# Optimization experiments

Measured on AMD Instinct MI355X. Metric: run time of the kernel, lower is better.

The kernel has to match this reference:

```python
import jax, jax.numpy as jnp
import numpy as np

N = 50000
E = 800000
D = 128          # in_dim == hidden_dim
EDGE_DIM = 1
H = 128          # hidden_dim


def setup_inputs() -> dict:
    key = jax.random.key(0)
    ks = jax.random.split(key, 16)
    inp = {
        "x": jax.random.normal(ks[0], (N, D), jnp.float32),
        "pos": jax.random.normal(ks[1], (N, 3), jnp.float32),
        "edge_index": jax.random.randint(ks[2], (2, E), 0, N, jnp.int64),
        "edge_attr": jax.random.normal(ks[3], (E, EDGE_DIM), jnp.float32),
        "s": jax.random.uniform(ks[4], (N,), jnp.float32),
    }
    # edge_mlp: Linear(2D+1+edge_dim -> H), SiLU, Linear(H -> H), SiLU
    e_in = 2 * D + 1 + EDGE_DIM
    def lin(k, fan_in, fan_out):
        lim = 1.0 / np.sqrt(fan_in)
        kw, kb = jax.random.split(k)
        W = jax.random.uniform(kw, (fan_in, fan_out), jnp.float32, -lim, lim)
        b = jax.random.uniform(kb, (fan_out,), jnp.float32, -lim, lim)
        return W, b
    inp["W_e1"], inp["b_e1"] = lin(ks[5], e_in, H)
    inp["W_e2"], inp["b_e2"] = lin(ks[6], H, H)
    # node_mlp: Linear(D+H -> H), SiLU, Linear(H -> D)
    inp["W_n1"], inp["b_n1"] = lin(ks[7], D + H, H)
    inp["W_n2"], inp["b_n2"] = lin(ks[8], H, D)
    # coord_mlp: Linear(H -> 1)
    inp["W_c"], inp["b_c"] = lin(ks[9], H, 1)
    return inp


def reference(x, pos, edge_index, edge_attr, s,
              W_e1, b_e1, W_e2, b_e2, W_n1, b_n1, W_n2, b_n2, W_c, b_c):
    src, dst = edge_index[0], edge_index[1]
    n = x.shape[0]

    # edge gather + relative geometry
    diff = pos[dst] - pos[src]                      # [E, 3]
    r2 = jnp.sum(diff * diff, axis=-1, keepdims=True)  # [E, 1]
    e_in = jnp.concatenate([x[dst], x[src], r2, edge_attr], axis=-1)  # [E, 2D+1+edge_dim]

    # edge MLP
    m = jax.nn.silu(e_in @ W_e1 + b_e1)
    m = jax.nn.silu(m @ W_e2 + b_e2)                # [E, H]

    # s-gate on source nodes
    m = m * s[src][:, None]

    # scatter-add aggregation with degree normalization
    m_sum = jax.ops.segment_sum(m, dst, num_segments=n)          # [N, H]
    deg = jax.ops.segment_sum(jnp.ones((m.shape[0], 1), m.dtype), dst, num_segments=n)
    deg = jnp.maximum(deg, 1.0)
    m_sum = m_sum / deg

    # node update
    h = jax.nn.silu(jnp.concatenate([x, m_sum], axis=-1) @ W_n1 + b_n1)
    x_out = h @ W_n2 + b_n2                         # [N, D]

    # coordinate update
    gamma = m @ W_c + b_c                           # [E, 1]
    coord_update = jax.ops.segment_sum(gamma * diff, dst, num_segments=n) / deg
    pos_out = pos + coord_update                    # [N, 3]
    return x_out, pos_out
```

## Files before the change

### kernel.cpp

```cpp
#include <hip/hip_runtime.h>
#include <hip/hip_bf16.h>

#define NN 50000
#define EE 800000
#define SCAN_BLOCKS 196

typedef __bf16 bf16x8_t __attribute__((ext_vector_type(8)));
typedef float f32x4_t __attribute__((ext_vector_type(4)));

__device__ __forceinline__ float silu_f(float v) {
    return v * __builtin_amdgcn_rcpf(1.0f + __expf(-v));
}

__global__ void prep_kernel(const float* __restrict__ x,
                            const float* __restrict__ We1,
                            const float* __restrict__ We2,
                            const float* __restrict__ Wn1,
                            const float* __restrict__ Wn2,
                            const int* __restrict__ eidx,
                            __bf16* __restrict__ xb,
                            __bf16* __restrict__ WyS,
                            __bf16* __restrict__ We2S,
                            __bf16* __restrict__ Wn1T,
                            __bf16* __restrict__ Wn2T,
                            int* __restrict__ hist) {
    int tid = blockIdx.x * blockDim.x + threadIdx.x;
    int np = gridDim.x * blockDim.x;
    const int NX = NN * 128 / 4;
    for (int i = tid; i < NX; i += np) {
        float4 v = ((const float4*)x)[i];
        __bf16* o = xb + (size_t)i * 4;
        o[0] = (__bf16)v.x; o[1] = (__bf16)v.y; o[2] = (__bf16)v.z; o[3] = (__bf16)v.w;
    }
    for (int i = tid; i < 256 * 128; i += np) {
        int k = i >> 7, n = i & 127;
        int h = (k < 128) ? n : (128 + n);
        int k2 = k & 127;
        WyS[(k2 >> 5) * 8192 + h * 32 + (k2 & 31)] = (__bf16)We1[i];
        Wn1T[n * 256 + k] = (__bf16)Wn1[i];
    }
    for (int i = tid; i < 128 * 128; i += np) {
        int k = i >> 7, n = i & 127;
        We2S[(k >> 5) * 4096 + n * 32 + (k & 31)] = (__bf16)We2[i];
        Wn2T[n * 128 + k] = (__bf16)Wn2[i];
    }
    for (int i = tid; i < EE; i += np) {
        atomicAdd(&hist[eidx[EE + i]], 1);
    }
}

__global__ __launch_bounds__(256, 4)
void ygemm_kernel(const __bf16* __restrict__ xb,
                  const __bf16* __restrict__ WyS,
                  float* __restrict__ y) {
    __shared__ __align__(16) __bf16 Abf[64 * 136];
    __shared__ __align__(16) __bf16 Wy[256 * 32];

    const int t = threadIdx.x;
    const int r0 = blockIdx.x * 64;
    const int w = t >> 6;
    const int lane = t & 63;
    const int m_ = lane & 15;
    const int q = lane >> 4;

#pragma unroll
    for (int i = 0; i < 4; ++i) {
        int id = t + 256 * i;
        int rl = id >> 4, c8 = (id & 15) * 8;
        int row = r0 + rl;
        uint4 v = (row < NN) ? *(const uint4*)(xb + (long)row * 128 + c8)
                             : make_uint4(0, 0, 0, 0);
        *(uint4*)(Abf + rl * 136 + c8) = v;
    }

    f32x4_t acc[16];
#pragma unroll
    for (int ct = 0; ct < 16; ++ct) acc[ct] = (f32x4_t){0.f, 0.f, 0.f, 0.f};

    const int wrow = t >> 2;
    const int pch = (t & 3) ^ ((wrow >> 1) & 3);
    const int wofs = wrow * 32 + pch * 8;
    const int rofs = m_ * 32 + (q ^ ((m_ >> 1) & 3)) * 8;

    uint4 v0 = *(const uint4*)(WyS + t * 8);
    uint4 v1 = *(const uint4*)(WyS + 2048 + t * 8);
    uint4 v2 = *(const uint4*)(WyS + 4096 + t * 8);
    uint4 v3 = *(const uint4*)(WyS + 6144 + t * 8);
#pragma unroll
    for (int ks = 0; ks < 4; ++ks) {
        __syncthreads();
        *(uint4*)(Wy + wofs) = v0;
        *(uint4*)(Wy + 64 * 32 + wofs) = v1;
        *(uint4*)(Wy + 128 * 32 + wofs) = v2;
        *(uint4*)(Wy + 192 * 32 + wofs) = v3;
        __syncthreads();
        if (ks < 3) {
            v0 = *(const uint4*)(WyS + (ks + 1) * 8192 + t * 8);
            v1 = *(const uint4*)(WyS + (ks + 1) * 8192 + 2048 + t * 8);
            v2 = *(const uint4*)(WyS + (ks + 1) * 8192 + 4096 + t * 8);
            v3 = *(const uint4*)(WyS + (ks + 1) * 8192 + 6144 + t * 8);
        }
        bf16x8_t a = *(const bf16x8_t*)(Abf + (w * 16 + m_) * 136 + ks * 32 + q * 8);
#pragma unroll
        for (int ct = 0; ct < 16; ++ct) {
            bf16x8_t b = *(const bf16x8_t*)(Wy + ct * (16 * 32) + rofs);
            acc[ct] = __builtin_amdgcn_mfma_f32_16x16x32_bf16(a, b, acc[ct], 0, 0, 0);
        }
    }
#pragma unroll
    for (int ct = 0; ct < 16; ++ct) {
        int c = ct * 16 + m_;
#pragma unroll
        for (int r = 0; r < 4; ++r) {
            int el = w * 16 + q * 4 + r;
            int row = r0 + el;
            if (row < NN) y[(long)row * 256 + c] = acc[ct][r];
        }
    }
}

__global__ void scan_a(const int* __restrict__ hist, int* __restrict__ bsum) {
    __shared__ int sh[256];
    int i = blockIdx.x * 256 + threadIdx.x;
    sh[threadIdx.x] = (i < NN) ? hist[i] : 0;
    __syncthreads();
    for (int s = 128; s > 0; s >>= 1) {
        if (threadIdx.x < s) sh[threadIdx.x] += sh[threadIdx.x + s];
        __syncthreads();
    }
    if (threadIdx.x == 0) bsum[blockIdx.x] = sh[0];
}

__global__ void scan_b(int* __restrict__ bsum) {
    __shared__ int sh[SCAN_BLOCKS];
    int t = threadIdx.x;
    if (t < SCAN_BLOCKS) sh[t] = bsum[t];
    __syncthreads();
    if (t == 0) {
        int acc = 0;
        for (int i = 0; i < SCAN_BLOCKS; ++i) { int v = sh[i]; sh[i] = acc; acc += v; }
    }
    __syncthreads();
    if (t < SCAN_BLOCKS) bsum[t] = sh[t];
}

__global__ void scan_c(const int* __restrict__ hist, const int* __restrict__ bsum,
                       int* __restrict__ off, int* __restrict__ cursor) {
    __shared__ int sh[256];
    int tx = threadIdx.x;
    int i = blockIdx.x * 256 + tx;
    int v = (i < NN) ? hist[i] : 0;
    sh[tx] = v;
    __syncthreads();
    for (int s = 1; s < 256; s <<= 1) {
        int add = (tx >= s) ? sh[tx - s] : 0;
        __syncthreads();
        sh[tx] += add;
        __syncthreads();
    }
    int excl = sh[tx] - v + bsum[blockIdx.x];
    if (i < NN) { off[i] = excl; cursor[i] = excl; }
    if (i == NN - 1) off[NN] = excl + v;
}

__global__ void scatter_kernel(const int* __restrict__ eidx,
                               const float* __restrict__ pos,
                               const float* __restrict__ eattr,
                               const float* __restrict__ s,
                               int* __restrict__ cursor,
                               float4* __restrict__ e_geo,
                               int2* __restrict__ e_nodes,
                               float2* __restrict__ e_gate) {
    int i = blockIdx.x * blockDim.x + threadIdx.x;
    if (i < EE) {
        int si = eidx[i];
        int di = eidx[EE + i];
        int p = atomicAdd(&cursor[di], 1);
        float dx = pos[di * 3 + 0] - pos[si * 3 + 0];
        float dy = pos[di * 3 + 1] - pos[si * 3 + 1];
        float dz = pos[di * 3 + 2] - pos[si * 3 + 2];
        e_geo[p] = make_float4(dx, dy, dz, dx * dx + dy * dy + dz * dz);
        e_nodes[p] = make_int2(si, di);
        e_gate[p] = make_float2(eattr[i], s[si]);
    }
}

__global__ __launch_bounds__(256, 3)
void edge_kernel(const float* __restrict__ y,
                 const float4* __restrict__ e_geo,
                 const int2* __restrict__ e_nodes,
                 const float2* __restrict__ e_gate,
                 const float* __restrict__ We1,
                 const float* __restrict__ be1,
                 const __bf16* __restrict__ We2S,
                 const float* __restrict__ be2,
                 const float* __restrict__ Wc,
                 const float* __restrict__ bc,
                 float* __restrict__ msum,
                 float* __restrict__ coordsum) {
    __shared__ __align__(16) __bf16 Wt[128 * 32];
    __shared__ __align__(16) __bf16 A2[128 * 136];
    __shared__ __align__(16) float4 s_pk[128];
    __shared__ float s_sg[128], s_g[128];
    __shared__ float s_diff[128 * 3];
    __shared__ int s_dst[128];

    float* Mf = (float*)A2;

    const int t = threadIdx.x;
    const int e0 = blockIdx.x * 128;
    const int w = t >> 6;
    const int lane = t & 63;
    const int m_ = lane & 15;
    const int q = lane >> 4;

    if (t < 128) {
        float4 g = e_geo[e0 + t];
        int2 nd = e_nodes[e0 + t];
        float2 gt = e_gate[e0 + t];
        s_diff[t * 3 + 0] = g.x; s_diff[t * 3 + 1] = g.y; s_diff[t * 3 + 2] = g.z;
        s_pk[t] = make_float4(g.w, gt.x, __int_as_float(nd.x), __int_as_float(nd.y));
        s_sg[t] = gt.y;
        s_dst[t] = nd.y;
    }
    __syncthreads();

    const int el0 = w * 16 + m_;
    const int el1 = 64 + w * 16 + m_;

    {
        const int cq = t & 31;
        const int c4 = cq * 4;
        const int eb = t >> 5;
        float4 b1 = *(const float4*)(be1 + c4);
        float4 w6 = *(const float4*)(We1 + 256 * 128 + c4);
        float4 w7 = *(const float4*)(We1 + 257 * 128 + c4);
#pragma unroll 4
        for (int i = 0; i < 16; ++i) {
            int e = eb + i * 8;
            float4 pk4 = s_pk[e];
            float r2 = pk4.x, ea = pk4.y;
            int sn = __float_as_int(pk4.z);
            int dn = __float_as_int(pk4.w);
            float4 ya = *(const float4*)(y + (long)dn * 256 + c4);
            float4 yb = *(const float4*)(y + (long)sn * 256 + 128 + c4);
            union { __bf16 h[4]; uint2 u2; } pk;
            pk.h[0] = (__bf16)silu_f(ya.x + yb.x + b1.x + r2 * w6.x + ea * w7.x);
            pk.h[1] = (__bf16)silu_f(ya.y + yb.y + b1.y + r2 * w6.y + ea * w7.y);
            pk.h[2] = (__bf16)silu_f(ya.z + yb.z + b1.z + r2 * w6.z + ea * w7.z);
            pk.h[3] = (__bf16)silu_f(ya.w + yb.w + b1.w + r2 * w6.w + ea * w7.w);
            *(uint2*)(A2 + e * 136 + c4) = pk.u2;
        }
    }

    f32x4_t acc[2][8];
#pragma unroll
    for (int et = 0; et < 2; ++et)
#pragma unroll
        for (int ot = 0; ot < 8; ++ot) acc[et][ot] = (f32x4_t){0.f, 0.f, 0.f, 0.f};

    const int wrow = t >> 2;
    const int pch = (t & 3) ^ ((wrow >> 1) & 3);
    const int wofs = wrow * 32 + pch * 8;
    const int rofs = m_ * 32 + (q ^ ((m_ >> 1) & 3)) * 8;

    uint4 w20 = *(const uint4*)(We2S + t * 8);
    uint4 w21 = *(const uint4*)(We2S + 2048 + t * 8);
#pragma unroll
    for (int ks = 0; ks < 4; ++ks) {
        __syncthreads();
        *(uint4*)(Wt + wofs) = w20;
        *(uint4*)(Wt + 64 * 32 + wofs) = w21;
        __syncthreads();
        if (ks < 3) {
            w20 = *(const uint4*)(We2S + (ks + 1) * 4096 + t * 8);
            w21 = *(const uint4*)(We2S + (ks + 1) * 4096 + 2048 + t * 8);
        }
        bf16x8_t af0 = *(const bf16x8_t*)(A2 + el0 * 136 + ks * 32 + q * 8);
        bf16x8_t af1 = *(const bf16x8_t*)(A2 + el1 * 136 + ks * 32 + q * 8);
#pragma unroll
        for (int ot = 0; ot < 8; ++ot) {
            bf16x8_t wf = *(const bf16x8_t*)(Wt + ot * (16 * 32) + rofs);
            acc[0][ot] = __builtin_amdgcn_mfma_f32_16x16x32_bf16(wf, af0, acc[0][ot], 0, 0, 0);
            acc[1][ot] = __builtin_amdgcn_mfma_f32_16x16x32_bf16(wf, af1, acc[1][ot], 0, 0, 0);
        }
    }

    {
        float sg0 = s_sg[el0], sg1 = s_sg[el1];
        float gp0 = 0.f, gp1 = 0.f;
#pragma unroll
        for (int ot = 0; ot < 8; ++ot) {
            int oc = ot * 16 + q * 4;
            float4 b2 = *(const float4*)(be2 + oc);
            float4 wc = *(const float4*)(Wc + oc);
            f32x4_t v0_ = acc[0][ot], v1_ = acc[1][ot];
            v0_[0] = silu_f(v0_[0] + b2.x) * sg0; v0_[1] = silu_f(v0_[1] + b2.y) * sg0;
            v0_[2] = silu_f(v0_[2] + b2.z) * sg0; v0_[3] = silu_f(v0_[3] + b2.w) * sg0;
            v1_[0] = silu_f(v1_[0] + b2.x) * sg1; v1_[1] = silu_f(v1_[1] + b2.y) * sg1;
            v1_[2] = silu_f(v1_[2] + b2.z) * sg1; v1_[3] = silu_f(v1_[3] + b2.w) * sg1;
            acc[0][ot] = v0_; acc[1][ot] = v1_;
            gp0 += v0_[0] * wc.x + v0_[1] * wc.y + v0_[2] * wc.z + v0_[3] * wc.w;
            gp1 += v1_[0] * wc.x + v1_[1] * wc.y + v1_[2] * wc.z + v1_[3] * wc.w;
        }
        gp0 += __shfl_xor(gp0, 16); gp0 += __shfl_xor(gp0, 32);
        gp1 += __shfl_xor(gp1, 16); gp1 += __shfl_xor(gp1, 32);
        if (q == 0) {
            float b0 = bc[0];
            s_g[el0] = gp0 + b0;
            s_g[el1] = gp1 + b0;
        }
    }
    __syncthreads();

    if (t < 24) {
        int ax = t % 3, ch = t / 3;
        int base = ch * 16;
        float run = 0.f;
        int cur = s_dst[base];
        for (int r = 0; r < 16; ++r) {
            int rr = base + r;
            int d = s_dst[rr];
            if (d != cur) {
                atomicAdd(&coordsum[cur * 3 + ax], run);
                run = 0.f; cur = d;
            }
            run += s_g[rr] * s_diff[rr * 3 + ax];
        }
        atomicAdd(&coordsum[cur * 3 + ax], run);
    }

#pragma unroll
    for (int ph = 0; ph < 2; ++ph) {
        int lr = w * 16 + m_;
#pragma unroll
        for (int ot = 0; ot < 8; ++ot)
            *(f32x4_t*)(Mf + lr * 132 + ot * 16 + q * 4) = acc[ph][ot];
        __syncthreads();
        {
            int c = t & 127;
            int half = t >> 7;
            int base = ph * 64 + half * 32;
            float run = 0.f;
            int cur = s_dst[base];
            for (int r = 0; r < 32; ++r) {
                int d = s_dst[base + r];
                if (d != cur) {
                    atomicAdd(&msum[(long)cur * 128 + c], run);
                    run = 0.f; cur = d;
                }
                run += Mf[(half * 32 + r) * 132 + c];
            }
            atomicAdd(&msum[(long)cur * 128 + c], run);
        }
        __syncthreads();
    }
}

__global__ __launch_bounds__(256, 2)
void node_kernel(const __bf16* __restrict__ xb,
                 const float* __restrict__ msum,
                 const int* __restrict__ off,
                 const __bf16* __restrict__ Wn1T,
                 const float* __restrict__ bn1,
                 const __bf16* __restrict__ Wn2T,
                 const float* __restrict__ bn2,
                 const float* __restrict__ pos,
                 const float* __restrict__ csum,
                 float* __restrict__ xout,
                 float* __restrict__ pout) {
    __shared__ __align__(16) __bf16 Abf[64 * 264];
    __shared__ __align__(16) __bf16 Wt[128 * 56];
    __shared__ __align__(16) __bf16 A2[64 * 136];

    const int t = threadIdx.x;
    const int r0 = blockIdx.x * 64;
    const int w = t >> 6;
    const int lane = t & 63;
    const int m_ = lane & 15;
    const int q = lane >> 4;

    if (t < 192) {
        int node = r0 + t / 3;
        if (node < NN) {
            int dg = off[node + 1] - off[node];
            float inv = 1.f / (float)(dg < 1 ? 1 : dg);
            int fl = node * 3 + t % 3;
            pout[fl] = pos[fl] + csum[fl] * inv;
        }
    }

    for (int i = 0; i < 8; ++i) {
        int id = t + 256 * i;
        int rl = id >> 5, ch = id & 31;
        int row = r0 + rl;
        int c8 = (ch & 15) * 8;
        union { __bf16 h[8]; uint4 u; } pk;
        if (row < NN) {
            if (ch < 16) {
                pk.u = *(const uint4*)(xb + (long)row * 128 + c8);
            } else {
                const float* mp = msum + (long)row * 128 + c8;
                int dg = off[row + 1] - off[row];
                float inv = 1.f / (float)(dg < 1 ? 1 : dg);
#pragma unroll
                for (int j = 0; j < 8; ++j) pk.h[j] = (__bf16)(mp[j] * inv);
            }
        } else {
            pk.u = make_uint4(0, 0, 0, 0);
        }
        *(uint4*)(Abf + rl * 264 + ((ch < 16) ? 0 : 128) + c8) = pk.u;
    }
    __syncthreads();

    f32x4_t acc[8];
#pragma unroll
    for (int ct = 0; ct < 8; ++ct) acc[ct] = (f32x4_t){0.f, 0.f, 0.f, 0.f};

    for (int ks = 0; ks < 8; ++ks) {
#pragma unroll
        for (int i = 0; i < 2; ++i) {
            int c = t + 256 * i;
            int n = c >> 2, ko = (c & 3) * 8;
            uint4 v = *(const uint4*)(Wn1T + n * 256 + ks * 32 + ko);
            *(uint4*)(Wt + n * 56 + ko) = v;
        }
        __syncthreads();
        bf16x8_t a = *(const bf16x8_t*)(Abf + (w * 16 + m_) * 264 + ks * 32 + q * 8);
#pragma unroll
        for (int ct = 0; ct < 8; ++ct) {
            bf16x8_t b = *(const bf16x8_t*)(Wt + (ct * 16 + m_) * 56 + q * 8);
            acc[ct] = __builtin_amdgcn_mfma_f32_16x16x32_bf16(a, b, acc[ct], 0, 0, 0);
        }
        __syncthreads();
    }
#pragma unroll
    for (int ct = 0; ct < 8; ++ct) {
        int c = ct * 16 + m_;
        float b1 = bn1[c];
#pragma unroll
        for (int r = 0; r < 4; ++r) {
            int el = w * 16 + q * 4 + r;
            float v = acc[ct][r] + b1;
            A2[el * 136 + c] = (__bf16)silu_f(v);
        }
    }
    __syncthreads();

#pragma unroll
    for (int ct = 0; ct < 8; ++ct) acc[ct] = (f32x4_t){0.f, 0.f, 0.f, 0.f};

    for (int ks = 0; ks < 4; ++ks) {
#pragma unroll
        for (int i = 0; i < 2; ++i) {
            int c = t + 256 * i;
            int n = c >> 2, ko = (c & 3) * 8;
            uint4 v = *(const uint4*)(Wn2T + n * 128 + ks * 32 + ko);
            *(uint4*)(Wt + n * 56 + ko) = v;
        }
        __syncthreads();
        bf16x8_t a = *(const bf16x8_t*)(A2 + (w * 16 + m_) * 136 + ks * 32 + q * 8);
#pragma unroll
        for (int ct = 0; ct < 8; ++ct) {
            bf16x8_t b = *(const bf16x8_t*)(Wt + (ct * 16 + m_) * 56 + q * 8);
            acc[ct] = __builtin_amdgcn_mfma_f32_16x16x32_bf16(a, b, acc[ct], 0, 0, 0);
        }
        __syncthreads();
    }
#pragma unroll
    for (int ct = 0; ct < 8; ++ct) {
        int c = ct * 16 + m_;
        float b2 = bn2[c];
#pragma unroll
        for (int r = 0; r < 4; ++r) {
            int el = w * 16 + q * 4 + r;
            int row = r0 + el;
            if (row < NN) xout[(long)row * 128 + c] = acc[ct][r] + b2;
        }
    }
}

extern "C" void kernel_launch(void* const* d_in, const int* in_sizes, int n_in,
                              void* d_out, int out_size, void* d_ws, size_t ws_size,
                              hipStream_t stream) {
    const float* x     = (const float*)d_in[0];
    const float* pos   = (const float*)d_in[1];
    const int*   eidx  = (const int*)d_in[2];
    const float* eattr = (const float*)d_in[3];
    const float* s     = (const float*)d_in[4];
    const float* We1   = (const float*)d_in[5];
    const float* be1   = (const float*)d_in[6];
    const float* We2   = (const float*)d_in[7];
    const float* be2   = (const float*)d_in[8];
    const float* Wn1   = (const float*)d_in[9];
    const float* bn1   = (const float*)d_in[10];
    const float* Wn2   = (const float*)d_in[11];
    const float* bn2   = (const float*)d_in[12];
    const float* Wc    = (const float*)d_in[13];
    const float* bc    = (const float*)d_in[14];

    char* ws = (char*)d_ws;
    __bf16* xb     = (__bf16*)(ws);
    __bf16* WyS    = (__bf16*)(ws + 12800000);
    __bf16* We2S   = (__bf16*)(ws + 12865536);
    __bf16* Wn1T   = (__bf16*)(ws + 12898304);
    __bf16* Wn2T   = (__bf16*)(ws + 12963840);
    float*  msum   = (float*)(ws + 12996608);
    float*  csum   = (float*)(ws + 38596608);
    int*    hist   = (int*)(ws + 39196608);
    int*    off    = (int*)(ws + 39396608);
    int*    cursor = (int*)(ws + 39596672);
    float4* e_geo  = (float4*)(ws + 39796736);
    int2*   e_nodes= (int2*)(ws + 52596736);
    float2* e_gate = (float2*)(ws + 58996736);
    int*    bsum   = (int*)(ws + 65396736);
    float*  y      = (float*)(ws + 65397760);

    float* xout = (float*)d_out;
    float* pout = xout + (size_t)NN * 128;

    hipMemsetAsync(ws + 12996608, 0, 26400000, stream);
    prep_kernel<<<1024, 256, 0, stream>>>(x, We1, We2, Wn1, Wn2, eidx,
                                          xb, WyS, We2S, Wn1T, Wn2T, hist);
    ygemm_kernel<<<(NN + 63) / 64, 256, 0, stream>>>(xb, WyS, y);
    scan_a<<<SCAN_BLOCKS, 256, 0, stream>>>(hist, bsum);
    scan_b<<<1, 256, 0, stream>>>(bsum);
    scan_c<<<SCAN_BLOCKS, 256, 0, stream>>>(hist, bsum, off, cursor);
    scatter_kernel<<<(EE + 255) / 256, 256, 0, stream>>>(eidx, pos, eattr, s, cursor,
                                                         e_geo, e_nodes, e_gate);
    edge_kernel<<<EE / 128, 256, 0, stream>>>(y, e_geo, e_nodes, e_gate,
                                              We1, be1, We2S, be2, Wc, bc,
                                              msum, csum);
    node_kernel<<<(NN + 63) / 64, 256, 0, stream>>>(xb, msum, off, Wn1T, bn1, Wn2T, bn2,
                                                    pos, csum, xout, pout);
}
```

Baseline: 412.1 us.

## Store node projections as split bf16 tables to halve edge gather traffic

The per-node first-layer projection y is now written as two bf16 arrays (dst half and src half) instead of one fp32 [N,256] array. The edge kernel gathers 8 bf16 values per thread with 16-byte loads, halving the bytes pulled per random row access. The ygemm kernel is also restructured to read x fragments straight from global memory with swapped MFMA operands, dropping the shared A tile, so each lane's outputs are contiguous along columns for packed bf16 stores. The cost is an extra bf16 rounding of the pre-activation partial sums, which reduces accuracy slightly.

```diff
diff --git a/kernel.cpp b/kernel.cpp
--- a/kernel.cpp
+++ b/kernel.cpp
@@ -11,6 +11,9 @@
 __device__ __forceinline__ float silu_f(float v) {
     return v * __builtin_amdgcn_rcpf(1.0f + __expf(-v));
 }
+
+__device__ __forceinline__ float bf_lo(unsigned u) { return __uint_as_float(u << 16); }
+__device__ __forceinline__ float bf_hi(unsigned u) { return __uint_as_float(u & 0xffff0000u); }
 
 __global__ void prep_kernel(const float* __restrict__ x,
                             const float* __restrict__ We1,
@@ -49,11 +52,11 @@
     }
 }
 
-__global__ __launch_bounds__(256, 4)
+__global__ __launch_bounds__(256, 3)
 void ygemm_kernel(const __bf16* __restrict__ xb,
                   const __bf16* __restrict__ WyS,
-                  float* __restrict__ y) {
-    __shared__ __align__(16) __bf16 Abf[64 * 136];
+                  __bf16* __restrict__ ya,
+                  __bf16* __restrict__ yb) {
     __shared__ __align__(16) __bf16 Wy[256 * 32];
 
     const int t = threadIdx.x;
@@ -63,25 +66,19 @@
     const int m_ = lane & 15;
     const int q = lane >> 4;
 
-#pragma unroll
-    for (int i = 0; i < 4; ++i) {
-        int id = t + 256 * i;
-        int rl = id >> 4, c8 = (id & 15) * 8;
-        int row = r0 + rl;
-        uint4 v = (row < NN) ? *(const uint4*)(xb + (long)row * 128 + c8)
-                             : make_uint4(0, 0, 0, 0);
-        *(uint4*)(Abf + rl * 136 + c8) = v;
-    }
+    const int node = r0 + w * 16 + m_;
+    const long nrow = (long)(node < NN ? node : NN - 1) * 128;
 
     f32x4_t acc[16];
 #pragma unroll
-    for (int ct = 0; ct < 16; ++ct) acc[ct] = (f32x4_t){0.f, 0.f, 0.f, 0.f};
+    for (int ot = 0; ot < 16; ++ot) acc[ot] = (f32x4_t){0.f, 0.f, 0.f, 0.f};
 
     const int wrow = t >> 2;
     const int pch = (t & 3) ^ ((wrow >> 1) & 3);
     const int wofs = wrow * 32 + pch * 8;
     const int rofs = m_ * 32 + (q ^ ((m_ >> 1) & 3)) * 8;
 
+    bf16x8_t xf = *(const bf16x8_t*)(xb + nrow + q * 8);
     uint4 v0 = *(const uint4*)(WyS + t * 8);
     uint4 v1 = *(const uint4*)(WyS + 2048 + t * 8);
     uint4 v2 = *(const uint4*)(WyS + 4096 + t * 8);
@@ -94,27 +91,33 @@
         *(uint4*)(Wy + 128 * 32 + wofs) = v2;
         *(uint4*)(Wy + 192 * 32 + wofs) = v3;
         __syncthreads();
+        bf16x8_t nxf;
         if (ks < 3) {
             v0 = *(const uint4*)(WyS + (ks + 1) * 8192 + t * 8);
             v1 = *(const uint4*)(WyS + (ks + 1) * 8192 + 2048 + t * 8);
             v2 = *(const uint4*)(WyS + (ks + 1) * 8192 + 4096 + t * 8);
             v3 = *(const uint4*)(WyS + (ks + 1) * 8192 + 6144 + t * 8);
-        }
-        bf16x8_t a = *(const bf16x8_t*)(Abf + (w * 16 + m_) * 136 + ks * 32 + q * 8);
-#pragma unroll
-        for (int ct = 0; ct < 16; ++ct) {
-            bf16x8_t b = *(const bf16x8_t*)(Wy + ct * (16 * 32) + rofs);
-            acc[ct] = __builtin_amdgcn_mfma_f32_16x16x32_bf16(a, b, acc[ct], 0, 0, 0);
-        }
-    }
-#pragma unroll
-    for (int ct = 0; ct < 16; ++ct) {
-        int c = ct * 16 + m_;
-#pragma unroll
-        for (int r = 0; r < 4; ++r) {
-            int el = w * 16 + q * 4 + r;
-            int row = r0 + el;
-            if (row < NN) y[(long)row * 256 + c] = acc[ct][r];
+            nxf = *(const bf16x8_t*)(xb + nrow + (ks + 1) * 32 + q * 8);
+        }
+#pragma unroll
+        for (int ot = 0; ot < 16; ++ot) {
+            bf16x8_t wf = *(const bf16x8_t*)(Wy + ot * (16 * 32) + rofs);
+            acc[ot] = __builtin_amdgcn_mfma_f32_16x16x32_bf16(wf, xf, acc[ot], 0, 0, 0);
+        }
+        if (ks < 3) xf = nxf;
+    }
+
+    if (node < NN) {
+#pragma unroll
+        for (int ot = 0; ot < 16; ++ot) {
+            union { __bf16 h[4]; uint2 u; } pk;
+            pk.h[0] = (__bf16)acc[ot][0];
+            pk.h[1] = (__bf16)acc[ot][1];
+            pk.h[2] = (__bf16)acc[ot][2];
+            pk.h[3] = (__bf16)acc[ot][3];
+            int col = (ot & 7) * 16 + q * 4;
+            __bf16* dst = (ot < 8 ? ya : yb) + (long)node * 128 + col;
+            *(uint2*)dst = pk.u;
         }
     }
 }
@@ -186,7 +189,8 @@
 }
 
 __global__ __launch_bounds__(256, 3)
-void edge_kernel(const float* __restrict__ y,
+void edge_kernel(const __bf16* __restrict__ ya,
+                 const __bf16* __restrict__ yb,
                  const float4* __restrict__ e_geo,
                  const int2* __restrict__ e_nodes,
                  const float2* __restrict__ e_gate,
@@ -229,27 +233,33 @@
     const int el1 = 64 + w * 16 + m_;
 
     {
-        const int cq = t & 31;
-        const int c4 = cq * 4;
-        const int eb = t >> 5;
-        float4 b1 = *(const float4*)(be1 + c4);
-        float4 w6 = *(const float4*)(We1 + 256 * 128 + c4);
-        float4 w7 = *(const float4*)(We1 + 257 * 128 + c4);
-#pragma unroll 4
-        for (int i = 0; i < 16; ++i) {
-            int e = eb + i * 8;
+        const int c8 = (t & 15) * 8;
+        const int eb = t >> 4;
+        float4 b1a = *(const float4*)(be1 + c8);
+        float4 b1b = *(const float4*)(be1 + c8 + 4);
+        float4 w6a = *(const float4*)(We1 + 256 * 128 + c8);
+        float4 w6b = *(const float4*)(We1 + 256 * 128 + c8 + 4);
+        float4 w7a = *(const float4*)(We1 + 257 * 128 + c8);
+        float4 w7b = *(const float4*)(We1 + 257 * 128 + c8 + 4);
+#pragma unroll 2
+        for (int i = 0; i < 8; ++i) {
+            int e = eb + i * 16;
             float4 pk4 = s_pk[e];
             float r2 = pk4.x, ea = pk4.y;
             int sn = __float_as_int(pk4.z);
             int dn = __float_as_int(pk4.w);
-            float4 ya = *(const float4*)(y + (long)dn * 256 + c4);
-            float4 yb = *(const float4*)(y + (long)sn * 256 + 128 + c4);
-            union { __bf16 h[4]; uint2 u2; } pk;
-            pk.h[0] = (__bf16)silu_f(ya.x + yb.x + b1.x + r2 * w6.x + ea * w7.x);
-            pk.h[1] = (__bf16)silu_f(ya.y + yb.y + b1.y + r2 * w6.y + ea * w7.y);
-            pk.h[2] = (__bf16)silu_f(ya.z + yb.z + b1.z + r2 * w6.z + ea * w7.z);
-            pk.h[3] = (__bf16)silu_f(ya.w + yb.w + b1.w + r2 * w6.w + ea * w7.w);
-            *(uint2*)(A2 + e * 136 + c4) = pk.u2;
+            uint4 av = *(const uint4*)(ya + (long)dn * 128 + c8);
+            uint4 bv = *(const uint4*)(yb + (long)sn * 128 + c8);
+            union { __bf16 h[8]; uint4 u; } pk;
+            pk.h[0] = (__bf16)silu_f(bf_lo(av.x) + bf_lo(bv.x) + b1a.x + r2 * w6a.x + ea * w7a.x);
+            pk.h[1] = (__bf16)silu_f(bf_hi(av.x) + bf_hi(bv.x) + b1a.y + r2 * w6a.y + ea * w7a.y);
+            pk.h[2] = (__bf16)silu_f(bf_lo(av.y) + bf_lo(bv.y) + b1a.z + r2 * w6a.z + ea * w7a.z);
+            pk.h[3] = (__bf16)silu_f(bf_hi(av.y) + bf_hi(bv.y) + b1a.w + r2 * w6a.w + ea * w7a.w);
+            pk.h[4] = (__bf16)silu_f(bf_lo(av.z) + bf_lo(bv.z) + b1b.x + r2 * w6b.x + ea * w7b.x);
+            pk.h[5] = (__bf16)silu_f(bf_hi(av.z) + bf_hi(bv.z) + b1b.y + r2 * w6b.y + ea * w7b.y);
+            pk.h[6] = (__bf16)silu_f(bf_lo(av.w) + bf_lo(bv.w) + b1b.z + r2 * w6b.z + ea * w7b.z);
+            pk.h[7] = (__bf16)silu_f(bf_hi(av.w) + bf_hi(bv.w) + b1b.w + r2 * w6b.w + ea * w7b.w);
+            *(uint4*)(A2 + e * 136 + c8) = pk.u;
         }
     }
 
@@ -514,7 +524,8 @@
     int2*   e_nodes= (int2*)(ws + 52596736);
     float2* e_gate = (float2*)(ws + 58996736);
     int*    bsum   = (int*)(ws + 65396736);
-    float*  y      = (float*)(ws + 65397760);
+    __bf16* ya     = (__bf16*)(ws + 65397760);
+    __bf16* yb     = (__bf16*)(ws + 78197760);
 
     float* xout = (float*)d_out;
     float* pout = xout + (size_t)NN * 128;
@@ -522,13 +533,13 @@
     hipMemsetAsync(ws + 12996608, 0, 26400000, stream);
     prep_kernel<<<1024, 256, 0, stream>>>(x, We1, We2, Wn1, Wn2, eidx,
                                           xb, WyS, We2S, Wn1T, Wn2T, hist);
-    ygemm_kernel<<<(NN + 63) / 64, 256, 0, stream>>>(xb, WyS, y);
+    ygemm_kernel<<<(NN + 63) / 64, 256, 0, stream>>>(xb, WyS, ya, yb);
     scan_a<<<SCAN_BLOCKS, 256, 0, stream>>>(hist, bsum);
     scan_b<<<1, 256, 0, stream>>>(bsum);
     scan_c<<<SCAN_BLOCKS, 256, 0, stream>>>(hist, bsum, off, cursor);
     scatter_kernel<<<(EE + 255) / 256, 256, 0, stream>>>(eidx, pos, eattr, s, cursor,
                                                          e_geo, e_nodes, e_gate);
-    edge_kernel<<<EE / 128, 256, 0, stream>>>(y, e_geo, e_nodes, e_gate,
+    edge_kernel<<<EE / 128, 256, 0, stream>>>(ya, yb, e_geo, e_nodes, e_gate,
                                               We1, be1, We2S, be2, Wc, bc,
                                               msum, csum);
     node_kernel<<<(NN + 63) / 64, 256, 0, stream>>>(xb, msum, off, Wn1T, bn1, Wn2T, bn2,
```

New measurement: 371.8 us. -9.8%, faster.
